# Kernel optimization log

Hardware: AMD Instinct MI355X
Metric: run time of the kernel (lower is better)

Reference implementation:

```python
import jax, jax.numpy as jnp
import numpy as np

N_NODES = 80000
N_EDGES = 1280000
D_NODE = 128
D_EDGE = 32
D_HID = 64
NEG_SLOPE = 0.2


def setup_inputs() -> dict:
    key = jax.random.key(0)
    ks = jax.random.split(key, 9)
    return {
        "node_features": jax.random.normal(ks[0], (N_NODES, D_NODE), dtype=jnp.float32),
        "edge_features": jax.random.normal(ks[1], (N_EDGES, D_EDGE), dtype=jnp.float32),
        "edge_index": jax.random.randint(ks[2], (2, N_EDGES), 0, N_NODES, dtype=jnp.int64),
        # params: w (node Linear), edgew (edge Linear), attn (3*hid -> 1)
        "w_w": jax.random.normal(ks[3], (D_NODE, D_HID), dtype=jnp.float32) / np.sqrt(D_NODE),
        "w_b": jax.random.normal(ks[4], (D_HID,), dtype=jnp.float32) * 0.01,
        "ew_w": jax.random.normal(ks[5], (D_EDGE, D_HID), dtype=jnp.float32) / np.sqrt(D_EDGE),
        "ew_b": jax.random.normal(ks[6], (D_HID,), dtype=jnp.float32) * 0.01,
        "a_w": jax.random.normal(ks[7], (3 * D_HID, 1), dtype=jnp.float32) / np.sqrt(3 * D_HID),
        "a_b": jax.random.normal(ks[8], (1,), dtype=jnp.float32) * 0.01,
    }


def reference(node_features, edge_features, edge_index, w_w, w_b, ew_w, ew_b, a_w, a_b):
    n_nodes = node_features.shape[0]
    h = node_features @ w_w + w_b              # [N, H]
    edge_h = edge_features @ ew_w + ew_b       # [E, H]
    tgt = edge_index[0]                        # target (softmax group) nodes i
    nbr = edge_index[1]                        # neighbor nodes j
    h_i = h[tgt]                               # [E, H] gather
    h_j = h[nbr]                               # [E, H] gather
    h_concat = jnp.concatenate([h_i, h_j, edge_h], axis=-1)  # [E, 3H]
    eij = jax.nn.leaky_relu(h_concat @ a_w + a_b, negative_slope=NEG_SLOPE)  # [E, 1]
    # scatter-softmax over edges grouped by target node (numerically stable)
    seg_max = jax.ops.segment_max(eij, tgt, num_segments=n_nodes)            # [N, 1]
    ex = jnp.exp(eij - seg_max[tgt])
    seg_sum = jax.ops.segment_sum(ex, tgt, num_segments=n_nodes)             # [N, 1]
    alpha = ex / seg_sum[tgt]                                                # [E, 1]
    # (dropout omitted for deterministic reference)
    message = alpha * h_j                                                    # [E, H]
    out = jax.ops.segment_sum(message, tgt, num_segments=n_nodes)            # [N, H]
    return jax.nn.elu(out)
```

## Files before the change

kernel.cpp:

```cpp
#include <hip/hip_runtime.h>
#include <math.h>

#define N_NODES 80000
#define N_EDGES 1280000
#define D_NODE  128
#define D_EDGE  32
#define D_HID   64
#define NEG_SLOPE 0.2f
#define NB 313
#define CAP 4608
#define BCNT_STRIDE 16
#define EB_BLK 512
#define EB_CHUNK 2048
#define EB_NCHUNK (N_EDGES / EB_CHUNK)

__device__ inline float waveReduceSum(float v) {
    #pragma unroll
    for (int o = 32; o > 0; o >>= 1) v += __shfl_xor(v, o);
    return v;
}
__device__ inline unsigned short f2bf(float f) {
    unsigned u = __float_as_uint(f);
    return (unsigned short)((u + 0x7FFF + ((u >> 16) & 1)) >> 16);
}
__device__ inline float bf2f(unsigned short v) {
    return __uint_as_float(((unsigned)v) << 16);
}

__global__ __launch_bounds__(256) void node_kernel(
        const float* __restrict__ nf, const float* __restrict__ w_w,
        const float* __restrict__ w_b, const float* __restrict__ a_w,
        unsigned short* __restrict__ hb, float* __restrict__ s1, float* __restrict__ s2) {
    __shared__ float Ws[D_HID * D_NODE];
    __shared__ float Xs[32][D_NODE];
    for (int i = threadIdx.x; i < D_NODE * D_HID; i += 256) {
        int k = i >> 6, d = i & 63;
        Ws[d * D_NODE + (((k >> 2) ^ (d & 7)) << 2) + (k & 3)] = w_w[i];
    }
    int lane = threadIdx.x & 63;
    int wv   = threadIdx.x >> 6;
    float wb = w_b[lane];
    float a1 = a_w[lane];
    float a2 = a_w[D_HID + lane];
    const float* wrow = &Ws[lane * D_NODE];
    const int nTiles = N_NODES / 32;
    for (int tile = blockIdx.x; tile < nTiles; tile += gridDim.x) {
        int n0 = tile * 32;
        __syncthreads();
        {
            const float4* src = (const float4*)(nf + (size_t)n0 * D_NODE);
            float4* dst = (float4*)&Xs[0][0];
            #pragma unroll
            for (int j = 0; j < 4; ++j)
                dst[threadIdx.x + 256 * j] = src[threadIdx.x + 256 * j];
        }
        __syncthreads();
        float acc[8] = {0.f, 0.f, 0.f, 0.f, 0.f, 0.f, 0.f, 0.f};
        const float* xs = &Xs[wv * 8][0];
        #pragma unroll 4
        for (int k4 = 0; k4 < 32; ++k4) {
            float4 w = *(const float4*)&wrow[(k4 ^ (lane & 7)) << 2];
            #pragma unroll
            for (int n = 0; n < 8; ++n) {
                float4 x = *(const float4*)&xs[n * D_NODE + (k4 << 2)];
                acc[n] += w.x * x.x + w.y * x.y + w.z * x.z + w.w * x.w;
            }
        }
        #pragma unroll
        for (int n = 0; n < 8; ++n) {
            int node = n0 + wv * 8 + n;
            float hv = acc[n] + wb;
            hb[(size_t)node * D_HID + lane] = f2bf(hv);
            float r1 = waveReduceSum(hv * a1);
            float r2 = waveReduceSum(hv * a2);
            if (lane == 0) { s1[node] = r1; s2[node] = r2; }
        }
    }
}

__global__ __launch_bounds__(EB_BLK) void edge_bin_kernel(
        const float* __restrict__ ef, const int* __restrict__ eidx,
        const float* __restrict__ s2v,
        const float* __restrict__ ew_w, const float* __restrict__ ew_b,
        const float* __restrict__ a_w, const float* __restrict__ a_b,
        int* __restrict__ bcnt, int2* __restrict__ binned) {
    __shared__ float cs[D_EDGE];
    __shared__ float bes;
    __shared__ int hist[NB], gbase[NB], rank[NB];
    __shared__ float sq [EB_CHUNK];
    __shared__ int   stg[EB_CHUNK];
    __shared__ int   snb[EB_CHUNK];
    int tid = threadIdx.x;
    if (tid < D_EDGE) {
        float s = 0.f;
        #pragma unroll
        for (int d = 0; d < D_HID; ++d) s += ew_w[tid * D_HID + d] * a_w[2 * D_HID + d];
        cs[tid] = s;
    } else if (tid == D_EDGE) {
        float s = 0.f;
        #pragma unroll
        for (int d = 0; d < D_HID; ++d) s += ew_b[d] * a_w[2 * D_HID + d];
        bes = s + a_b[0];
    }
    int qd = tid >> 2;
    int j  = tid & 3;
    for (int c = blockIdx.x; c < EB_NCHUNK; c += gridDim.x) {
        for (int i = tid; i < NB; i += EB_BLK) { hist[i] = 0; rank[i] = 0; }
        __syncthreads();
        int e0 = c * EB_CHUNK;
        #pragma unroll
        for (int k = 0; k < 4; ++k) {
            int idx = k * EB_BLK + tid;
            int e = e0 + idx;
            int tg = eidx[e];
            int nb = eidx[N_EDGES + e];
            stg[idx] = tg;
            snb[idx] = nb;
            sq [idx] = bes + s2v[nb];
            atomicAdd(&hist[tg >> 8], 1);
        }
        __syncthreads();
        #pragma unroll 2
        for (int rr = 0; rr < EB_CHUNK / 128; ++rr) {
            int idx = rr * 128 + qd;
            int e = e0 + idx;
            const float4* f4 = (const float4*)ef;
            float4 fa = f4[(size_t)e * 8 + j];
            float4 fb = f4[(size_t)e * 8 + 4 + j];
            const float4 c1 = *(const float4*)&cs[j * 4];
            const float4 c2 = *(const float4*)&cs[16 + j * 4];
            float p = fa.x * c1.x + fa.y * c1.y + fa.z * c1.z + fa.w * c1.w
                    + fb.x * c2.x + fb.y * c2.y + fb.z * c2.z + fb.w * c2.w;
            p += __shfl_xor(p, 1);
            p += __shfl_xor(p, 2);
            if (j == 0) sq[idx] += p;
        }
        __syncthreads();
        for (int i = tid; i < NB; i += EB_BLK) {
            int cc = hist[i];
            if (cc) gbase[i] = i * CAP + atomicAdd(&bcnt[i * BCNT_STRIDE], cc);
        }
        __syncthreads();
        #pragma unroll
        for (int k = 0; k < 4; ++k) {
            int idx = k * EB_BLK + tid;
            int tg = stg[idx];
            int b  = tg >> 8;
            int r  = atomicAdd(&rank[b], 1);
            binned[gbase[b] + r] = make_int2(((tg & 255) << 17) | snb[idx],
                                             __float_as_int(sq[idx]));
        }
        __syncthreads();
    }
}

__global__ __launch_bounds__(512) void bucket_scan_kernel(
        const int* __restrict__ bcnt, int* __restrict__ bbase,
        int* __restrict__ node_off) {
    __shared__ int buf[512];
    int v = (threadIdx.x < NB) ? bcnt[threadIdx.x * BCNT_STRIDE] : 0;
    buf[threadIdx.x] = v;
    __syncthreads();
    for (int ofs = 1; ofs < 512; ofs <<= 1) {
        int t = (threadIdx.x >= (unsigned)ofs) ? buf[threadIdx.x - ofs] : 0;
        __syncthreads();
        buf[threadIdx.x] += t;
        __syncthreads();
    }
    if (threadIdx.x < NB) bbase[threadIdx.x] = buf[threadIdx.x] - v;
    if (threadIdx.x == NB - 1) bbase[NB] = buf[threadIdx.x];
    if (threadIdx.x == 0) node_off[N_NODES] = N_EDGES;
}

__global__ __launch_bounds__(256) void bucket_csr_kernel(
        const int* __restrict__ bcnt, const int* __restrict__ bbase,
        const int2* __restrict__ binned, int* __restrict__ node_off,
        int2* __restrict__ pay2) {
    __shared__ int nhist[256], buf[256], ncur[256];
    int b = blockIdx.x;
    int in0  = b * CAP;
    int cnt  = bcnt[b * BCNT_STRIDE];
    int out0 = bbase[b];
    nhist[threadIdx.x] = 0;
    __syncthreads();
    for (int i = threadIdx.x; i < cnt; i += 256)
        atomicAdd(&nhist[binned[in0 + i].x >> 17], 1);
    __syncthreads();
    int v = nhist[threadIdx.x];
    buf[threadIdx.x] = v;
    __syncthreads();
    for (int ofs = 1; ofs < 256; ofs <<= 1) {
        int t = (threadIdx.x >= (unsigned)ofs) ? buf[threadIdx.x - ofs] : 0;
        __syncthreads();
        buf[threadIdx.x] += t;
        __syncthreads();
    }
    int excl = buf[threadIdx.x] - v;
    int n = b * 256 + (int)threadIdx.x;
    if (n < N_NODES) node_off[n] = out0 + excl;
    ncur[threadIdx.x] = excl;
    __syncthreads();
    for (int i = threadIdx.x; i < cnt; i += 256) {
        int2 p = binned[in0 + i];
        int r = atomicAdd(&ncur[p.x >> 17], 1);
        pay2[out0 + r] = make_int2(p.x & 0x1FFFF, p.y);
    }
}

__global__ __launch_bounds__(256) void accum_kernel(
        const int* __restrict__ node_off, const int2* __restrict__ pay2,
        const float* __restrict__ s1, const unsigned short* __restrict__ hb,
        float* __restrict__ out) {
    __shared__ float exs[4][64];
    __shared__ int   nbs[4][64];
    int wv = threadIdx.x >> 6, lane = threadIdx.x & 63;
    int node = blockIdx.x * 4 + wv;
    if (node >= N_NODES) return;
    int base = node_off[node];
    int cnt  = node_off[node + 1] - base;
    if (cnt == 0) { out[(size_t)node * D_HID + lane] = 0.f; return; }
    float s1i = s1[node];
    float sumex = 0.f, acc = 0.f;
    for (int c0 = 0; c0 < cnt; c0 += 64) {
        int i = c0 + lane;
        int nc = min(64, cnt - c0);
        float exv = 0.f; int nb = 0;
        if (i < cnt) {
            int2 p = pay2[base + i];
            nb = p.x;
            float s = s1i + __int_as_float(p.y);
            s = (s > 0.f) ? s : NEG_SLOPE * s;
            exv = __expf(s);
        }
        sumex += exv;
        exs[wv][lane] = exv;
        nbs[wv][lane] = nb;
        for (int j = 0; j < nc; ++j) {
            acc += exs[wv][j] * bf2f(hb[(size_t)nbs[wv][j] * D_HID + lane]);
        }
    }
    sumex = waveReduceSum(sumex);
    float o = acc / sumex;
    out[(size_t)node * D_HID + lane] = (o > 0.f) ? o : (__expf(o) - 1.f);
}

extern "C" void kernel_launch(void* const* d_in, const int* in_sizes, int n_in,
                              void* d_out, int out_size, void* d_ws, size_t ws_size,
                              hipStream_t stream) {
    const float* nf   = (const float*)d_in[0];
    const float* ef   = (const float*)d_in[1];
    const int*   eidx = (const int*)d_in[2];
    const float* w_w  = (const float*)d_in[3];
    const float* w_b  = (const float*)d_in[4];
    const float* ew_w = (const float*)d_in[5];
    const float* ew_b = (const float*)d_in[6];
    const float* a_w  = (const float*)d_in[7];
    const float* a_b  = (const float*)d_in[8];
    float* out = (float*)d_out;

    char* ws = (char*)d_ws;
    size_t o = 0;
    auto alloc = [&](size_t bytes) -> void* {
        void* p = ws + o;
        o = (o + bytes + 255) & ~(size_t)255;
        return p;
    };
    unsigned short* hb  = (unsigned short*)alloc((size_t)N_NODES * D_HID * 2);
    float* s1       = (float*)alloc((size_t)N_NODES * 4);
    float* s2       = (float*)alloc((size_t)N_NODES * 4);
    int*   bcnt     = (int*)alloc((size_t)NB * BCNT_STRIDE * 4);
    int*   bbase    = (int*)alloc((size_t)(NB + 1) * 4);
    int*   node_off = (int*)alloc((size_t)(N_NODES + 1) * 4);
    int2*  binned   = (int2*)alloc((size_t)NB * CAP * 8);
    int2*  pay2     = (int2*)alloc((size_t)N_EDGES * 8);

    hipMemsetAsync(bcnt, 0, (size_t)NB * BCNT_STRIDE * 4, stream);

    node_kernel<<<1250, 256, 0, stream>>>(nf, w_w, w_b, a_w, hb, s1, s2);
    edge_bin_kernel<<<EB_NCHUNK, EB_BLK, 0, stream>>>(ef, eidx, s2, ew_w, ew_b, a_w, a_b, bcnt, binned);
    bucket_scan_kernel<<<1, 512, 0, stream>>>(bcnt, bbase, node_off);
    bucket_csr_kernel<<<NB, 256, 0, stream>>>(bcnt, bbase, binned, node_off, pay2);
    accum_kernel<<<(N_NODES + 3) / 4, 256, 0, stream>>>(node_off, pay2, s1, hb, out);
}
```

Baseline: 162.2 us.

## Process four nodes per wave with 16-lane groups and vectorized bf16 gathers

After: 156.5 us. 3.5% less time.

```diff
diff --git a/kernel.cpp b/kernel.cpp
--- a/kernel.cpp
+++ b/kernel.cpp
@@ -211,37 +211,50 @@
         const int* __restrict__ node_off, const int2* __restrict__ pay2,
         const float* __restrict__ s1, const unsigned short* __restrict__ hb,
         float* __restrict__ out) {
-    __shared__ float exs[4][64];
-    __shared__ int   nbs[4][64];
-    int wv = threadIdx.x >> 6, lane = threadIdx.x & 63;
-    int node = blockIdx.x * 4 + wv;
-    if (node >= N_NODES) return;
+    int tid = threadIdx.x;
+    int wv = tid >> 6, lane = tid & 63;
+    int grp = lane >> 4, li = lane & 15;
+    int node = blockIdx.x * 16 + wv * 4 + grp;
     int base = node_off[node];
     int cnt  = node_off[node + 1] - base;
-    if (cnt == 0) { out[(size_t)node * D_HID + lane] = 0.f; return; }
     float s1i = s1[node];
-    float sumex = 0.f, acc = 0.f;
-    for (int c0 = 0; c0 < cnt; c0 += 64) {
-        int i = c0 + lane;
-        int nc = min(64, cnt - c0);
-        float exv = 0.f; int nb = 0;
+    float ax = 0.f, ay = 0.f, az = 0.f, aw = 0.f;
+    float sumex = 0.f;
+    for (int c0 = 0; c0 < cnt; c0 += 16) {
+        int i = c0 + li;
+        int nc = min(16, cnt - c0);
+        float exv = 0.f; int nbv = 0;
         if (i < cnt) {
             int2 p = pay2[base + i];
-            nb = p.x;
+            nbv = p.x;
             float s = s1i + __int_as_float(p.y);
             s = (s > 0.f) ? s : NEG_SLOPE * s;
             exv = __expf(s);
         }
         sumex += exv;
-        exs[wv][lane] = exv;
-        nbs[wv][lane] = nb;
         for (int j = 0; j < nc; ++j) {
-            acc += exs[wv][j] * bf2f(hb[(size_t)nbs[wv][j] * D_HID + lane]);
-        }
-    }
-    sumex = waveReduceSum(sumex);
-    float o = acc / sumex;
-    out[(size_t)node * D_HID + lane] = (o > 0.f) ? o : (__expf(o) - 1.f);
+            float w  = __shfl(exv, grp * 16 + j);
+            int   nb = __shfl(nbv, grp * 16 + j);
+            uint2 v = *(const uint2*)&hb[(size_t)nb * D_HID + li * 4];
+            ax += w * bf2f((unsigned short)(v.x & 0xFFFF));
+            ay += w * bf2f((unsigned short)(v.x >> 16));
+            az += w * bf2f((unsigned short)(v.y & 0xFFFF));
+            aw += w * bf2f((unsigned short)(v.y >> 16));
+        }
+    }
+    #pragma unroll
+    for (int o = 8; o > 0; o >>= 1) sumex += __shfl_xor(sumex, o);
+    float4 o4;
+    if (cnt == 0) {
+        o4 = make_float4(0.f, 0.f, 0.f, 0.f);
+    } else {
+        o4.x = ax / sumex; o4.y = ay / sumex; o4.z = az / sumex; o4.w = aw / sumex;
+        o4.x = (o4.x > 0.f) ? o4.x : (__expf(o4.x) - 1.f);
+        o4.y = (o4.y > 0.f) ? o4.y : (__expf(o4.y) - 1.f);
+        o4.z = (o4.z > 0.f) ? o4.z : (__expf(o4.z) - 1.f);
+        o4.w = (o4.w > 0.f) ? o4.w : (__expf(o4.w) - 1.f);
+    }
+    ((float4*)out)[(size_t)node * 16 + li] = o4;
 }
 
 extern "C" void kernel_launch(void* const* d_in, const int* in_sizes, int n_in,
@@ -280,5 +293,5 @@
     edge_bin_kernel<<<EB_NCHUNK, EB_BLK, 0, stream>>>(ef, eidx, s2, ew_w, ew_b, a_w, a_b, bcnt, binned);
     bucket_scan_kernel<<<1, 512, 0, stream>>>(bcnt, bbase, node_off);
     bucket_csr_kernel<<<NB, 256, 0, stream>>>(bcnt, bbase, binned, node_off, pay2);
-    accum_kernel<<<(N_NODES + 3) / 4, 256, 0, stream>>>(node_off, pay2, s1, hb, out);
-}
+    accum_kernel<<<N_NODES / 16, 256, 0, stream>>>(node_off, pay2, s1, hb, out);
+}
```
